# Optimization experiments

Measured on AMD Instinct MI355X. Metric: run time of the kernel, lower is better.

Reference implementation:

```python
import jax, jax.numpy as jnp
import numpy as np

IN_F, OUT_F = 512, 512
GRID_SIZE, SPLINE_ORDER = 5, 3
K = GRID_SIZE + SPLINE_ORDER  # 8 basis functions
B, S = 8, 1024


def setup_inputs() -> dict:
    key = jax.random.key(0)
    k1, k2, k3, k4, k5 = jax.random.split(key, 5)
    return {
        "x": jax.random.normal(k1, (B, S, IN_F), dtype=jnp.float32),
        "coeff": jax.random.normal(k2, (OUT_F, IN_F, K), dtype=jnp.float32),
        "scale_base": jax.random.normal(k3, (OUT_F, IN_F), dtype=jnp.float32) * 0.1,
        "scale_spline": jax.random.normal(k4, (OUT_F, IN_F), dtype=jnp.float32),
        "base_bias": jax.random.normal(k5, (OUT_F, IN_F), dtype=jnp.float32),
    }


def reference(x, coeff, scale_base, scale_spline, base_bias):
    batch = x.shape[0]
    in_f = x.shape[-1]
    k = coeff.shape[-1]

    xc = jnp.clip(x.reshape(-1, in_f), -1.0, 1.0)      # (N, in)
    base = jax.nn.silu(xc)                              # (N, in)

    # polynomial basis recurrence: b0 = 1, b1 = x, b_i = 2*x*b_{i-1} - 1
    bases = [jnp.ones_like(xc), xc]
    for _ in range(2, k):
        bases.append(2.0 * xc * bases[-1] - 1.0)
    basis = jnp.stack(bases[:k], axis=-1)               # (N, in, K)

    # spline[n,o] = sum_{i,k} scale_spline[o,i]*coeff[o,i,k]*basis[n,i,k]
    w_spline = scale_spline[..., None] * coeff          # (out, in, K)
    spline_term = jnp.einsum('nik,oik->no', basis, w_spline)
    base_term = base @ scale_base.T                     # (N, out)
    out = base_term + spline_term + jnp.sum(base_bias, axis=1)  # (N, out)

    out = out.reshape(batch, -1, base_bias.shape[0])    # (B, S, out)
    if out.shape[-2] == 1:
        out = out[..., 0, :]
    return out
```

## Files before the change

### kernel.cpp

```cpp
#include <hip/hip_runtime.h>
#include <hip/hip_bf16.h>

#define IN_FEAT 512
#define OUT_FEAT 512
#define NTOK 8192
#define KDIM 4096

typedef short bf16x8 __attribute__((ext_vector_type(8)));
typedef float f32x16 __attribute__((ext_vector_type(16)));

static __device__ inline short f2bf(float f) {
    union { float f; unsigned u; } v; v.f = f;
    unsigned u = v.u;
    u += 0x7fffu + ((u >> 16) & 1u);
    return (short)(u >> 16);
}

static __device__ inline unsigned cvtpk(float lo, float hi) {
    unsigned r;
    asm("v_cvt_pk_bf16_f32 %0, %1, %2" : "=v"(r) : "v"(lo), "v"(hi));
    return r;
}

static __device__ inline bf16x8 gen_chunk(float xv) {
    float xc = fminf(fmaxf(xv, -1.f), 1.f);
    float e  = __expf(-xc);
    float bse = xc * __builtin_amdgcn_rcpf(1.f + e);
    float b2 = 2.f * xc * xc - 1.f;
    float b3 = 2.f * xc * b2 - 1.f;
    float b4 = 2.f * xc * b3 - 1.f;
    float b5 = 2.f * xc * b4 - 1.f;
    float b6 = 2.f * xc * b5 - 1.f;
    float b7 = 2.f * xc * b6 - 1.f;
    union { uint4 u; bf16x8 v; } r;
    r.u.x = cvtpk(bse, xc);
    r.u.y = cvtpk(b2, b3);
    r.u.z = cvtpk(b4, b5);
    r.u.w = cvtpk(b6, b7);
    return r.v;
}

static __device__ inline void gload_lds16(const short* g, short* l) {
    __builtin_amdgcn_global_load_lds(
        (const __attribute__((address_space(1))) unsigned int*)g,
        (__attribute__((address_space(3))) unsigned int*)l,
        16, 0, 0);
}

__global__ __launch_bounds__(256) void kan_prep(
    const float* __restrict__ coeff, const float* __restrict__ scale_base,
    const float* __restrict__ scale_spline, const float* __restrict__ base_bias,
    short* __restrict__ Wb, float* __restrict__ bias)
{
    int o = blockIdx.x;
    int tid = threadIdx.x;
    float local = 0.f;
#pragma unroll
    for (int rep = 0; rep < 2; ++rep) {
        int i = tid + rep * 256;
        size_t oi = (size_t)o * IN_FEAT + i;
        const float4* c4 = (const float4*)(coeff + oi * 8);
        float4 ca = c4[0], cb = c4[1];
        float ss = scale_spline[oi];
        float sb = scale_base[oi];
        local += base_bias[oi] + ss * ca.x;
        bf16x8 w;
        w[0] = f2bf(sb);
        w[1] = f2bf(ss * ca.y); w[2] = f2bf(ss * ca.z); w[3] = f2bf(ss * ca.w);
        w[4] = f2bf(ss * cb.x); w[5] = f2bf(ss * cb.y); w[6] = f2bf(ss * cb.z);
        w[7] = f2bf(ss * cb.w);
        *(bf16x8*)(Wb + (size_t)o * KDIM + (size_t)i * 8) = w;
    }
    __shared__ float red[4];
    for (int off = 32; off > 0; off >>= 1) local += __shfl_down(local, off, 64);
    int lane = tid & 63, wv = tid >> 6;
    if (lane == 0) red[wv] = local;
    __syncthreads();
    if (tid == 0) bias[o] = red[0] + red[1] + red[2] + red[3];
}

__global__ __launch_bounds__(256, 2) void kan_gemm17(
    const float* __restrict__ x, const short* __restrict__ Wb,
    const float* __restrict__ bias, float* __restrict__ out)
{
    __shared__ __align__(16) short POOL[32768];
    short* Bs = POOL;

    int tid = threadIdx.x;
    int bid = blockIdx.x;
    int j8 = bid & 7, t = bid >> 3;
    int mb = j8 * 8 + (t & 7);
    int nb = t >> 3;
    int m0 = mb * 128, o0 = nb * 64;

    int lane = tid & 63, wv = tid >> 6;
    int kk = wv;
    int l31 = lane & 31, half = lane >> 5;

    f32x16 acc[4][2];
#pragma unroll
    for (int a = 0; a < 4; ++a)
#pragma unroll
        for (int b = 0; b < 2; ++b) acc[a][b] = (f32x16)0.f;

    int rl2 = lane >> 5, q32 = lane & 31;
    const short* pB[8];
#pragma unroll
    for (int c = 0; c < 8; ++c) {
        int row = wv * 16 + c * 2 + rl2;
        int g = q32 ^ (row & 31);
        pB[c] = Wb + (size_t)(o0 + row) * KDIM + (size_t)g * 8;
    }
    int bd0 = wv * 16 * 256;

    const float* xp0 = x + (size_t)(m0 + l31) * IN_FEAT + kk * 8;

    int ofr[4];
#pragma unroll
    for (int j = 0; j < 4; ++j)
        ofr[j] = l31 * 256 + (((kk * 8 + 2 * j + half) ^ l31) * 8);

#define MFMA_(A, B, C) __builtin_amdgcn_mfma_f32_32x32x16_bf16(A, B, C, 0, 0, 0)

#define GENSEL(Qa, Qb, J) ((J) == 0 ? (half ? (Qa).y : (Qa).x)                \
                         : (J) == 1 ? (half ? (Qa).w : (Qa).z)                \
                         : (J) == 2 ? (half ? (Qb).y : (Qb).x)                \
                                    : (half ? (Qb).w : (Qb).z))

#define STAGE(BUF, IT, Q0a, Q0b, Q1a, Q1b, Q2a, Q2b, Q3a, Q3b)                \
    {                                                                         \
        short* bd_ = Bs + (BUF) * 16384 + bd0;                                \
        const size_t bo_ = (size_t)(IT) * 256;                                \
        _Pragma("unroll")                                                     \
        for (int c_ = 0; c_ < 8; ++c_)                                        \
            gload_lds16(pB[c_] + bo_, bd_ + c_ * 512);                        \
        const float* xq_ = xp0 + (size_t)(IT) * 32;                           \
        Q0a = *(const float4*)(xq_);          Q0b = *(const float4*)(xq_ + 4);          \
        Q1a = *(const float4*)(xq_ + 16384);  Q1b = *(const float4*)(xq_ + 16388);      \
        Q2a = *(const float4*)(xq_ + 32768);  Q2b = *(const float4*)(xq_ + 32772);      \
        Q3a = *(const float4*)(xq_ + 49152);  Q3b = *(const float4*)(xq_ + 49156);      \
    }

#define COMPUTE(CUR, Q0a, Q0b, Q1a, Q1b, Q2a, Q2b, Q3a, Q3b)                  \
    {                                                                         \
        const short* Bc_ = Bs + (CUR) * 16384;                                \
        _Pragma("unroll")                                                     \
        for (int j_ = 0; j_ < 4; ++j_) {                                      \
            bf16x8 b0_ = *(const bf16x8*)(Bc_ + ofr[j_]);                     \
            bf16x8 b1_ = *(const bf16x8*)(Bc_ + ofr[j_] + 8192);              \
            bf16x8 a0_ = gen_chunk(GENSEL(Q0a, Q0b, j_));                     \
            bf16x8 a1_ = gen_chunk(GENSEL(Q1a, Q1b, j_));                     \
            bf16x8 a2_ = gen_chunk(GENSEL(Q2a, Q2b, j_));                     \
            bf16x8 a3_ = gen_chunk(GENSEL(Q3a, Q3b, j_));                     \
            acc[0][0] = MFMA_(a0_, b0_, acc[0][0]); acc[0][1] = MFMA_(a0_, b1_, acc[0][1]); \
            acc[1][0] = MFMA_(a1_, b0_, acc[1][0]); acc[1][1] = MFMA_(a1_, b1_, acc[1][1]); \
            acc[2][0] = MFMA_(a2_, b0_, acc[2][0]); acc[2][1] = MFMA_(a2_, b1_, acc[2][1]); \
            acc[3][0] = MFMA_(a3_, b0_, acc[3][0]); acc[3][1] = MFMA_(a3_, b1_, acc[3][1]); \
        }                                                                     \
    }

    float4 A0a, A0b, A1a, A1b, A2a, A2b, A3a, A3b;
    float4 B0a, B0b, B1a, B1b, B2a, B2b, B3a, B3b;

    STAGE(0, 0, A0a, A0b, A1a, A1b, A2a, A2b, A3a, A3b);
    for (int jj = 0; jj < 8; ++jj) {
        __syncthreads();
        STAGE(1, 2 * jj + 1, B0a, B0b, B1a, B1b, B2a, B2b, B3a, B3b);
        COMPUTE(0, A0a, A0b, A1a, A1b, A2a, A2b, A3a, A3b);
        __syncthreads();
        if (jj < 7)
            STAGE(0, 2 * jj + 2, A0a, A0b, A1a, A1b, A2a, A2b, A3a, A3b);
        COMPUTE(1, B0a, B0b, B1a, B1b, B2a, B2b, B3a, B3b);
    }
#undef STAGE
#undef COMPUTE
#undef GENSEL
#undef MFMA_

    float* rbuf = (float*)POOL;
#pragma unroll
    for (int p = 0; p < 2; ++p) {
        __syncthreads();
        if (kk >= 2) {
            float* s_ = rbuf + (size_t)(kk - 2) * 4224 + lane * 66;
#pragma unroll
            for (int fm = 0; fm < 2; ++fm)
#pragma unroll
                for (int fn = 0; fn < 2; ++fn)
#pragma unroll
                    for (int r = 0; r < 16; ++r)
                        s_[(fm * 2 + fn) * 16 + r] = acc[2 * p + fm][fn][r];
        }
        __syncthreads();
        if (kk < 2) {
            const float* s_ = rbuf + (size_t)kk * 4224 + lane * 66;
#pragma unroll
            for (int fm = 0; fm < 2; ++fm)
#pragma unroll
                for (int fn = 0; fn < 2; ++fn)
#pragma unroll
                    for (int r = 0; r < 16; ++r)
                        acc[2 * p + fm][fn][r] += s_[(fm * 2 + fn) * 16 + r];
        }
        __syncthreads();
        if (kk == 1) {
            float* s_ = rbuf + lane * 66;
#pragma unroll
            for (int fm = 0; fm < 2; ++fm)
#pragma unroll
                for (int fn = 0; fn < 2; ++fn)
#pragma unroll
                    for (int r = 0; r < 16; ++r)
                        s_[(fm * 2 + fn) * 16 + r] = acc[2 * p + fm][fn][r];
        }
        __syncthreads();
        if (kk == 0) {
            const float* s_ = rbuf + lane * 66;
#pragma unroll
            for (int fn = 0; fn < 2; ++fn) {
                int o = o0 + fn * 32 + l31;
                float bv = bias[o];
#pragma unroll
                for (int fm = 0; fm < 2; ++fm) {
#pragma unroll
                    for (int r = 0; r < 16; ++r) {
                        float v = acc[2 * p + fm][fn][r] + s_[(fm * 2 + fn) * 16 + r] + bv;
                        int token = m0 + (2 * p + fm) * 32 + (r & 3) + 8 * (r >> 2) + 4 * half;
                        out[(size_t)token * OUT_FEAT + o] = v;
                    }
                }
            }
        }
    }
}

extern "C" void kernel_launch(void* const* d_in, const int* in_sizes, int n_in,
                              void* d_out, int out_size, void* d_ws, size_t ws_size,
                              hipStream_t stream) {
    const float* x            = (const float*)d_in[0];
    const float* coeff        = (const float*)d_in[1];
    const float* scale_base   = (const float*)d_in[2];
    const float* scale_spline = (const float*)d_in[3];
    const float* base_bias    = (const float*)d_in[4];
    float* out = (float*)d_out;

    short* Wb   = (short*)d_ws;
    float* bias = (float*)((char*)d_ws + (size_t)OUT_FEAT * KDIM * 2);

    kan_prep<<<OUT_FEAT, 256, 0, stream>>>(coeff, scale_base, scale_spline, base_bias, Wb, bias);
    kan_gemm17<<<(NTOK / 128) * (OUT_FEAT / 64), 256, 0, stream>>>(x, Wb, bias, out);
}
```

Before: 126.5 us.

## Fuse weight prep and GEMM into one cooperative kernel with grid sync

Merges the weight-preparation kernel and the GEMM kernel into a single cooperative launch of 512 blocks that run the prep phase, synchronise the whole grid, then run the GEMM. It also remaps which output rows each block prepares and changes the block-to-tile mapping so each block's GEMM tile lines up with the weights it just wrote. The aim is to remove the second launch and the gap between kernels, at the cost of a grid-wide barrier and a dependence on all 512 blocks being co-resident. If the cooperative launch fails, it falls back to the two separate kernels.

```diff
diff --git a/kernel.cpp b/kernel.cpp
--- a/kernel.cpp
+++ b/kernel.cpp
@@ -1,5 +1,7 @@
 #include <hip/hip_runtime.h>
 #include <hip/hip_bf16.h>
+#include <hip/hip_cooperative_groups.h>
+namespace cg = cooperative_groups;
 
 #define IN_FEAT 512
 #define OUT_FEAT 512
@@ -47,12 +49,12 @@
         16, 0, 0);
 }
 
-__global__ __launch_bounds__(256) void kan_prep(
+static __device__ __forceinline__ void prep_body(
     const float* __restrict__ coeff, const float* __restrict__ scale_base,
     const float* __restrict__ scale_spline, const float* __restrict__ base_bias,
-    short* __restrict__ Wb, float* __restrict__ bias)
-{
-    int o = blockIdx.x;
+    short* __restrict__ Wb, float* __restrict__ bias, float* red)
+{
+    int o = (blockIdx.x & 7) * 64 + (blockIdx.x >> 3);
     int tid = threadIdx.x;
     float local = 0.f;
 #pragma unroll
@@ -71,7 +73,6 @@
         w[7] = f2bf(ss * cb.w);
         *(bf16x8*)(Wb + (size_t)o * KDIM + (size_t)i * 8) = w;
     }
-    __shared__ float red[4];
     for (int off = 32; off > 0; off >>= 1) local += __shfl_down(local, off, 64);
     int lane = tid & 63, wv = tid >> 6;
     if (lane == 0) red[wv] = local;
@@ -79,18 +80,16 @@
     if (tid == 0) bias[o] = red[0] + red[1] + red[2] + red[3];
 }
 
-__global__ __launch_bounds__(256, 2) void kan_gemm17(
+static __device__ __forceinline__ void gemm_body(
     const float* __restrict__ x, const short* __restrict__ Wb,
-    const float* __restrict__ bias, float* __restrict__ out)
-{
-    __shared__ __align__(16) short POOL[32768];
+    const float* __restrict__ bias, float* __restrict__ out, short* POOL)
+{
     short* Bs = POOL;
 
     int tid = threadIdx.x;
     int bid = blockIdx.x;
-    int j8 = bid & 7, t = bid >> 3;
-    int mb = j8 * 8 + (t & 7);
-    int nb = t >> 3;
+    int k8 = bid & 7, t = bid >> 3;
+    int mb = t, nb = k8;
     int m0 = mb * 128, o0 = nb * 64;
 
     int lane = tid & 63, wv = tid >> 6;
@@ -111,7 +110,7 @@
         int g = q32 ^ (row & 31);
         pB[c] = Wb + (size_t)(o0 + row) * KDIM + (size_t)g * 8;
     }
-    int bd0 = wv * 16 * 256;
+    int bd0 = wv * 4096;
 
     const float* xp0 = x + (size_t)(m0 + l31) * IN_FEAT + kk * 8;
 
@@ -234,6 +233,35 @@
     }
 }
 
+__global__ __launch_bounds__(256, 2) void kan_fused(
+    const float* __restrict__ x, const float* __restrict__ coeff,
+    const float* __restrict__ scale_base, const float* __restrict__ scale_spline,
+    const float* __restrict__ base_bias, short* __restrict__ Wb,
+    float* __restrict__ bias, float* __restrict__ out)
+{
+    __shared__ __align__(16) short POOL[32768];
+    prep_body(coeff, scale_base, scale_spline, base_bias, Wb, bias, (float*)POOL);
+    cg::this_grid().sync();
+    gemm_body(x, Wb, bias, out, POOL);
+}
+
+__global__ __launch_bounds__(256) void kan_prep_fb(
+    const float* __restrict__ coeff, const float* __restrict__ scale_base,
+    const float* __restrict__ scale_spline, const float* __restrict__ base_bias,
+    short* __restrict__ Wb, float* __restrict__ bias)
+{
+    __shared__ float red[4];
+    prep_body(coeff, scale_base, scale_spline, base_bias, Wb, bias, red);
+}
+
+__global__ __launch_bounds__(256, 2) void kan_gemm_fb(
+    const float* __restrict__ x, const short* __restrict__ Wb,
+    const float* __restrict__ bias, float* __restrict__ out)
+{
+    __shared__ __align__(16) short POOL[32768];
+    gemm_body(x, Wb, bias, out, POOL);
+}
+
 extern "C" void kernel_launch(void* const* d_in, const int* in_sizes, int n_in,
                               void* d_out, int out_size, void* d_ws, size_t ws_size,
                               hipStream_t stream) {
@@ -247,6 +275,16 @@
     short* Wb   = (short*)d_ws;
     float* bias = (float*)((char*)d_ws + (size_t)OUT_FEAT * KDIM * 2);
 
-    kan_prep<<<OUT_FEAT, 256, 0, stream>>>(coeff, scale_base, scale_spline, base_bias, Wb, bias);
-    kan_gemm17<<<(NTOK / 128) * (OUT_FEAT / 64), 256, 0, stream>>>(x, Wb, bias, out);
-}
+    void* args[] = { (void*)&x, (void*)&coeff, (void*)&scale_base,
+                     (void*)&scale_spline, (void*)&base_bias,
+                     (void*)&Wb, (void*)&bias, (void*)&out };
+    hipError_t e = hipLaunchCooperativeKernel((const void*)kan_fused,
+                                              dim3(512), dim3(256),
+                                              args, 0, stream);
+    if (e != hipSuccess) {
+        (void)hipGetLastError();
+        kan_prep_fb<<<512, 256, 0, stream>>>(coeff, scale_base, scale_spline,
+                                             base_bias, Wb, bias);
+        kan_gemm_fb<<<512, 256, 0, stream>>>(x, Wb, bias, out);
+    }
+}
```

Measured after the change: 181.3 us. 1.43x slower.
